# Kernel tuning notes

Measured on AMD Instinct MI355X. Metric: run time of the kernel, lower is better.

The kernel has to match this reference:

```python
import jax, jax.numpy as jnp
import numpy as np

B, E, H, V, T = 64, 512, 1024, 32000, 31  # T = max_len - 1


def _lstm_step(x, h, c, Wx, Wh, b):
    # Keras LSTM with activation=None (linear), recurrent_activation=sigmoid, gate order i,f,g,o
    z = x @ Wx + h @ Wh + b
    i, f, g, o = jnp.split(z, 4, axis=-1)
    c_new = jax.nn.sigmoid(f) * c + jax.nn.sigmoid(i) * g  # g is linear (activation=None)
    h_new = jax.nn.sigmoid(o) * c_new                      # linear activation on cell output
    return h_new, c_new


def setup_inputs() -> dict:
    key = jax.random.key(0)
    k = jax.random.split(key, 6)
    def gl(kk, shape, fan_in):
        return jax.random.normal(kk, shape, dtype=jnp.float32) / np.float32(np.sqrt(fan_in))
    return {
        "inp": jax.random.normal(k[0], (B, 1, E), dtype=jnp.float32),
        "Wx1": gl(k[1], (E, 4 * H), E),
        "Wh1": gl(k[2], (H, 4 * H), H),
        "b1": jnp.zeros((4 * H,), jnp.float32),
        "Wx2": gl(k[3], (H, 4 * H), H),
        "Wh2": gl(k[4], (H, 4 * H), H),
        "b2": jnp.zeros((4 * H,), jnp.float32),
        "Wd": gl(k[5], (H, V), H),
        "bd": jnp.zeros((V,), jnp.float32),
    }


def reference(inp, Wx1, Wh1, b1, Wx2, Wh2, b2, Wd, bd):
    Bk = inp.shape[0]
    h = jnp.zeros((Bk, H), inp.dtype)
    c = jnp.zeros((Bk, H), inp.dtype)

    # encoder LSTM over the (length-1) input sequence, zero initial state
    def enc(carry, x):
        h, c = carry
        h, c = _lstm_step(x, h, c, Wx1, Wh1, b1)
        return (h, c), None
    (h, c), _ = jax.lax.scan(enc, (h, c), jnp.swapaxes(inp, 0, 1))  # time-major (T_in,B,E)

    key = jax.random.key(1234)

    # decode loop: lstm_rest consumes its own previous output (== previous state_h)
    def dec(carry, t):
        h, c = carry
        h2, c2 = _lstm_step(h, h, c, Wx2, Wh2, b2)
        logp = jax.nn.log_softmax(h2 @ Wd + bd, axis=-1)  # Dense(softmax) -> Categorical(probs)
        probs = jnp.exp(logp)
        kk = jax.random.fold_in(key, t)
        sample = jax.random.categorical(kk, logp, axis=-1)                    # dist.sample()
        log_prob = jnp.take_along_axis(logp, sample[:, None], axis=1)[:, 0]   # dist.log_prob
        ent = -jnp.sum(probs * logp, axis=-1)                                 # dist.entropy
        return (h2, c2), (sample, log_prob, ent)

    (h, c), (msg, lp, ent) = jax.lax.scan(dec, (h, c), jnp.arange(T))

    def pad(a):  # (T,B) -> (B,T) then concat zeros along axis 1 -> (B,2T)
        a = a.T
        return jnp.concatenate([a, jnp.zeros_like(a)], axis=1)

    return pad(msg), pad(lp), pad(ent), h
```

## Files before the change

kernel.cpp:

```cpp
#include <hip/hip_runtime.h>
#include <stdint.h>
#include <math.h>

#define B_DIM 64
#define E_DIM 512
#define H_DIM 1024
#define V_DIM 32000
#define T_STEPS 31
#define GATES 4096
#define OUT_COLS 62
#define NCHUNK 125
#define STOT 32
#define NTPAIR 16
#define NBLK2 (NTPAIR * NCHUNK)

#define RNG_PARTITIONABLE 1

typedef _Float16 half8 __attribute__((ext_vector_type(8)));
typedef float floatx4 __attribute__((ext_vector_type(4)));

__device__ __forceinline__ void tf_round(uint32_t& x0, uint32_t& x1, int r) {
  x0 += x1;
  x1 = (x1 << r) | (x1 >> (32 - r));
  x1 ^= x0;
}

__device__ __forceinline__ void threefry2x32(uint32_t k0, uint32_t k1,
                                             uint32_t& x0, uint32_t& x1) {
  uint32_t k2 = k0 ^ k1 ^ 0x1BD11BDAu;
  x0 += k0; x1 += k1;
  tf_round(x0,x1,13); tf_round(x0,x1,15); tf_round(x0,x1,26); tf_round(x0,x1,6);
  x0 += k1; x1 += k2 + 1u;
  tf_round(x0,x1,17); tf_round(x0,x1,29); tf_round(x0,x1,16); tf_round(x0,x1,24);
  x0 += k2; x1 += k0 + 2u;
  tf_round(x0,x1,13); tf_round(x0,x1,15); tf_round(x0,x1,26); tf_round(x0,x1,6);
  x0 += k0; x1 += k1 + 3u;
  tf_round(x0,x1,17); tf_round(x0,x1,29); tf_round(x0,x1,16); tf_round(x0,x1,24);
  x0 += k1; x1 += k2 + 4u;
  tf_round(x0,x1,13); tf_round(x0,x1,15); tf_round(x0,x1,26); tf_round(x0,x1,6);
  x0 += k2; x1 += k0 + 5u;
}

__global__ void zero_kernel(float* __restrict__ o, int n) {
  int i = blockIdx.x * blockDim.x + threadIdx.x;
  if (i < n) o[i] = 0.0f;
}

__global__ void copy_kernel(const float* __restrict__ a, float* __restrict__ o, int n) {
  int i = blockIdx.x * blockDim.x + threadIdx.x;
  if (i < n) o[i] = a[i];
}

__global__ __launch_bounds__(256)
void repack_w(const float* __restrict__ Wa, const float* __restrict__ Wb,
              _Float16* __restrict__ pk, int N) {
  int gw = blockIdx.x * 4 + (threadIdx.x >> 6);
  int total = (N >> 4) * STOT;
  if (gw >= total) return;
  int nt = gw >> 5, s = gw & 31;
  int lane = threadIdx.x & 63;
  int quad = lane >> 4, lm = lane & 15;
  int col = nt * 16 + lm;
  half8 hi, lo;
#pragma unroll
  for (int j = 0; j < 8; ++j) {
    int row = s * 32 + quad * 8 + j;
    float v = Wa[(size_t)row * N + col];
    if (Wb) v += Wb[(size_t)row * N + col];
    _Float16 h = (_Float16)v;
    hi[j] = h;
    lo[j] = (_Float16)(v - (float)h);
  }
  _Float16* o = pk + ((size_t)(nt * 32 + s) * 2) * 512 + lane * 8;
  *(half8*)o = hi;
  *(half8*)(o + 512) = lo;
}

#define LOAD_FRAGS(s_, A_, B_)                                              \
  {                                                                         \
    _Pragma("unroll")                                                       \
    for (int mt = 0; mt < 4; ++mt) {                                        \
      const half8* ap = Apk + ((size_t)(mt * 32 + (s_)) * 2) * 64 + lane;   \
      A_[mt][0] = ap[0];                                                    \
      A_[mt][1] = ap[64];                                                   \
    }                                                                       \
    _Pragma("unroll")                                                       \
    for (int nt = 0; nt < 4; ++nt) {                                        \
      const half8* bp =                                                     \
          Wpk + ((size_t)((nt0 + nt) * 32 + (s_)) * 2) * 64 + lane;         \
      B_[nt][0] = bp[0];                                                    \
      B_[nt][1] = bp[64];                                                   \
    }                                                                       \
  }

#define DO_MFMA(A_, B_)                                                     \
  {                                                                         \
    _Pragma("unroll")                                                       \
    for (int mt = 0; mt < 4; ++mt) {                                        \
      _Pragma("unroll")                                                     \
      for (int nt = 0; nt < 4; ++nt) {                                      \
        acc[mt][nt] = __builtin_amdgcn_mfma_f32_16x16x32_f16(               \
            A_[mt][0], B_[nt][0], acc[mt][nt], 0, 0, 0);                    \
        acc[mt][nt] = __builtin_amdgcn_mfma_f32_16x16x32_f16(               \
            A_[mt][1], B_[nt][0], acc[mt][nt], 0, 0, 0);                    \
        acc[mt][nt] = __builtin_amdgcn_mfma_f32_16x16x32_f16(               \
            A_[mt][0], B_[nt][1], acc[mt][nt], 0, 0, 0);                    \
      }                                                                     \
    }                                                                       \
  }

__global__ __launch_bounds__(256, 1)
void mfma_gemm(const half8* __restrict__ Apk, const half8* __restrict__ Wpk,
               float* __restrict__ P, int N) {
  const int w = threadIdx.x >> 6;
  const int lane = threadIdx.x & 63;
  const int schunk = STOT / gridDim.y;
  const int s0 = blockIdx.y * schunk;
  const int send = s0 + schunk;
  const int nt0 = blockIdx.x * 16 + w * 4;

  floatx4 acc[4][4] = {};
  half8 a0[4][2], b0[4][2], a1[4][2], b1[4][2];

  LOAD_FRAGS(s0, a0, b0);
  for (int s = s0; s < send; s += 2) {
    LOAD_FRAGS(s + 1, a1, b1);
    DO_MFMA(a0, b0);
    if (s + 2 < send) LOAD_FRAGS(s + 2, a0, b0);
    DO_MFMA(a1, b1);
  }

  const int row0 = (lane >> 4) * 4;
  const int colb = blockIdx.x * 256 + w * 64 + (lane & 15);
  float* Pb = P + (size_t)blockIdx.y * 64 * N;
#pragma unroll
  for (int mt = 0; mt < 4; ++mt)
#pragma unroll
    for (int nt = 0; nt < 4; ++nt)
#pragma unroll
      for (int r = 0; r < 4; ++r)
        Pb[(size_t)(mt * 16 + row0 + r) * N + colb + nt * 16] = acc[mt][nt][r];
}

__global__ __launch_bounds__(512, 2)
void mfma_logits_fused(const half8* __restrict__ hpkA, const half8* __restrict__ Wpk,
                       const float* __restrict__ bd,
                       float* __restrict__ pm, float* __restrict__ ps,
                       float* __restrict__ pt2, float* __restrict__ pbest,
                       float* __restrict__ plb, int* __restrict__ pbi) {
  const int p = blockIdx.x;
  const int g = (p & 7) * 250 + (p >> 3);
  const int tpair = g & 15;
  const int chunk = g >> 4;

  const int tid = threadIdx.x;
  const int w4 = tid >> 6;
  const int th = w4 >> 2;
  const int w  = w4 & 3;
  const int lane = tid & 63;
  const int lm = lane & 15, q = lane >> 4;
  const int t = tpair * 2 + th;
  const bool active = (t < T_STEPS);
  const int nt0 = chunk * 16 + w * 4;

  floatx4 acc[4][4] = {};

  if (active) {
    const half8* Apk = hpkA + (size_t)(t + 1) * 16384;
    half8 a0[4][2], b0[4][2], a1[4][2], b1[4][2];

    LOAD_FRAGS(0, a0, b0);
    for (int s = 0; s < STOT; s += 2) {
      LOAD_FRAGS(s + 1, a1, b1);
      DO_MFMA(a0, b0);
      if (s + 2 < STOT) LOAD_FRAGS(s + 2, a0, b0);
      DO_MFMA(a1, b1);
    }
  }

  __shared__ float redM[2][4][64];
  __shared__ float redS[2][4][64], redT[2][4][64], redBV[2][4][64], redBL[2][4][64];
  __shared__ int   redBI[2][4][64];

  const int colb = chunk * 256 + w * 64 + lm;
  float M[4][4];

  if (active) {
    float bdv[4];
#pragma unroll
    for (int nt = 0; nt < 4; ++nt) bdv[nt] = bd[colb + nt * 16];
#pragma unroll
    for (int mt = 0; mt < 4; ++mt)
#pragma unroll
      for (int nt = 0; nt < 4; ++nt)
#pragma unroll
        for (int r = 0; r < 4; ++r) acc[mt][nt][r] += bdv[nt];

#pragma unroll
    for (int mt = 0; mt < 4; ++mt) {
#pragma unroll
      for (int r = 0; r < 4; ++r) {
        float m = fmaxf(fmaxf(acc[mt][0][r], acc[mt][1][r]),
                        fmaxf(acc[mt][2][r], acc[mt][3][r]));
#pragma unroll
        for (int off = 1; off <= 8; off <<= 1) m = fmaxf(m, __shfl_xor(m, off));
        if (lm == 0) redM[th][w][mt * 16 + q * 4 + r] = m;
      }
    }
  }
  __syncthreads();

  if (active) {
#pragma unroll
    for (int mt = 0; mt < 4; ++mt)
#pragma unroll
      for (int r = 0; r < 4; ++r) {
        int b = mt * 16 + q * 4 + r;
        M[mt][r] = fmaxf(fmaxf(redM[th][0][b], redM[th][1][b]),
                         fmaxf(redM[th][2][b], redM[th][3][b]));
      }

    uint32_t tk0 = 0u, tk1 = (uint32_t)t;
    threefry2x32(0u, 1234u, tk0, tk1);

#pragma unroll
    for (int mt = 0; mt < 4; ++mt) {
#pragma unroll
      for (int r = 0; r < 4; ++r) {
        const int b = mt * 16 + q * 4 + r;
        const float Mrow = M[mt][r];
        float s = 0.f, t2 = 0.f, bv = -INFINITY, bl = 0.f;
        int bi = 0x7fffffff;
#pragma unroll
        for (int nt = 0; nt < 4; ++nt) {
          float l = acc[mt][nt][r];
          int v = colb + nt * 16;
          float e = __expf(l - Mrow);
          s += e;
          t2 += e * l;
          uint32_t j = (uint32_t)(b * V_DIM + v);
#if RNG_PARTITIONABLE
          uint32_t y0 = 0u, y1 = j;
          threefry2x32(tk0, tk1, y0, y1);
          uint32_t bits = y0 ^ y1;
#else
          const uint32_t half = (uint32_t)(B_DIM * V_DIM / 2);
          uint32_t y0, y1;
          if (j < half) { y0 = j; y1 = j + half; } else { y0 = j - half; y1 = j; }
          threefry2x32(tk0, tk1, y0, y1);
          uint32_t bits = (j < half) ? y0 : y1;
#endif
          float u = __uint_as_float((bits >> 9) | 0x3f800000u) - 1.0f;
          u = fmaxf(u, 1.17549435e-38f);
          float g2 = -__logf(-__logf(u));
          float val = l + g2;
          if (val > bv || (val == bv && v < bi)) { bv = val; bi = v; bl = l; }
        }
#pragma unroll
        for (int off = 1; off <= 8; off <<= 1) {
          s  += __shfl_xor(s, off);
          t2 += __shfl_xor(t2, off);
          float ob = __shfl_xor(bv, off);
          int   oi = __shfl_xor(bi, off);
          float ol = __shfl_xor(bl, off);
          if (ob > bv || (ob == bv && oi < bi)) { bv = ob; bi = oi; bl = ol; }
        }
        if (lm == 0) {
          redS[th][w][b] = s; redT[th][w][b] = t2;
          redBV[th][w][b] = bv; redBI[th][w][b] = bi; redBL[th][w][b] = bl;
        }
      }
    }
  }
  __syncthreads();

  if (active && w == 0) {
    int b = lane;
    float Mg = fmaxf(fmaxf(redM[th][0][b], redM[th][1][b]),
                     fmaxf(redM[th][2][b], redM[th][3][b]));
    float S  = redS[th][0][b] + redS[th][1][b] + redS[th][2][b] + redS[th][3][b];
    float T2 = redT[th][0][b] + redT[th][1][b] + redT[th][2][b] + redT[th][3][b];
    float Bv = redBV[th][0][b]; int BI = redBI[th][0][b]; float Bl = redBL[th][0][b];
#pragma unroll
    for (int ww = 1; ww < 4; ++ww) {
      if (redBV[th][ww][b] > Bv || (redBV[th][ww][b] == Bv && redBI[th][ww][b] < BI)) {
        Bv = redBV[th][ww][b]; BI = redBI[th][ww][b]; Bl = redBL[th][ww][b];
      }
    }
    size_t o = ((size_t)t * B_DIM + b) * NCHUNK + chunk;
    pm[o] = Mg; ps[o] = S; pt2[o] = T2; pbest[o] = Bv; plb[o] = Bl;
    pbi[o] = BI;
  }
}
#undef LOAD_FRAGS
#undef DO_MFMA

__global__ __launch_bounds__(256, 2)
void gemm64_kernel(const float* __restrict__ A, const float* __restrict__ W,
                   float* __restrict__ P, int K, int N) {
  const int vt = blockIdx.x;
  const int ks = blockIdx.y;
  const int kchunk = K / gridDim.y;
  const int kbase = ks * kchunk;
  const int v0 = vt * 256;

  __shared__ float As[32][68];
  __shared__ float Ws[32][256];

  float acc[8][8];
#pragma unroll
  for (int i = 0; i < 8; i++)
#pragma unroll
    for (int j = 0; j < 8; j++) acc[i][j] = 0.0f;

  const int tid = threadIdx.x;
  const int cg4 = (tid & 31) * 4;
  const int rg4 = (tid >> 5) * 4;

  for (int k0 = kbase; k0 < kbase + kchunk; k0 += 32) {
    __syncthreads();
    {
      int b  = tid >> 3;
      int f4 = tid & 7;
      const float* Ab = A + (size_t)b * K + k0 + f4 * 4;
      float4 a0 = *(const float4*)Ab;
      float4 a1 = *(const float4*)(Ab + (size_t)32 * K);
      int kk0 = f4 * 4;
      As[kk0+0][b] = a0.x; As[kk0+1][b] = a0.y; As[kk0+2][b] = a0.z; As[kk0+3][b] = a0.w;
      As[kk0+0][b+32] = a1.x; As[kk0+1][b+32] = a1.y; As[kk0+2][b+32] = a1.z; As[kk0+3][b+32] = a1.w;
    }
#pragma unroll
    for (int p = 0; p < 8; p++) {
      int idx = tid + p * 256;
      int row = idx >> 6, c4 = idx & 63;
      *(float4*)&Ws[row][c4 * 4] =
          *(const float4*)(W + (size_t)(k0 + row) * N + v0 + c4 * 4);
    }
    __syncthreads();

#pragma unroll 8
    for (int kk = 0; kk < 32; kk++) {
      float4 a0 = *(const float4*)&As[kk][rg4];
      float4 a1 = *(const float4*)&As[kk][32 + rg4];
      float4 w0 = *(const float4*)&Ws[kk][cg4];
      float4 w1 = *(const float4*)&Ws[kk][128 + cg4];
      float av[8] = {a0.x, a0.y, a0.z, a0.w, a1.x, a1.y, a1.z, a1.w};
      float wv[8] = {w0.x, w0.y, w0.z, w0.w, w1.x, w1.y, w1.z, w1.w};
#pragma unroll
      for (int i = 0; i < 8; i++)
#pragma unroll
        for (int j = 0; j < 8; j++)
          acc[i][j] = fmaf(av[i], wv[j], acc[i][j]);
    }
  }

  const size_t base = (size_t)ks * 64 * N;
#pragma unroll
  for (int i = 0; i < 8; i++) {
    int row = (i < 4) ? (rg4 + i) : (32 + rg4 + i - 4);
    float4 s0 = make_float4(acc[i][0], acc[i][1], acc[i][2], acc[i][3]);
    float4 s1 = make_float4(acc[i][4], acc[i][5], acc[i][6], acc[i][7]);
    *(float4*)(P + base + (size_t)row * N + v0 + cg4) = s0;
    *(float4*)(P + base + (size_t)row * N + v0 + 128 + cg4) = s1;
  }
}

__global__ void gates_kernel(const float* __restrict__ zp, int ksplit,
                             const float* __restrict__ bias,
                             const float* __restrict__ c_in,
                             float* __restrict__ h_out, float* __restrict__ c_out,
                             _Float16* __restrict__ hpk) {
  int tid = blockIdx.x * blockDim.x + threadIdx.x;
  if (tid >= B_DIM * H_DIM) return;
  int b = tid >> 10, j = tid & 1023;
  float zi = bias[j], zf = bias[j + 1024], zg = bias[j + 2048], zo = bias[j + 3072];
  const float* Pb = zp + (size_t)b * GATES;
  for (int p = 0; p < ksplit; p++) {
    const float* P = Pb + (size_t)p * B_DIM * GATES;
    zi += P[j]; zf += P[j + 1024]; zg += P[j + 2048]; zo += P[j + 3072];
  }
  float cp = c_in ? c_in[tid] : 0.0f;
  float si = 1.0f / (1.0f + expf(-zi));
  float sf = 1.0f / (1.0f + expf(-zf));
  float so = 1.0f / (1.0f + expf(-zo));
  float c = sf * cp + si * zg;
  c_out[tid] = c;
  float hv = so * c;
  h_out[tid] = hv;

  int mt = b >> 4, lm = b & 15;
  int s = j >> 5, quad = (j >> 3) & 3, jj = j & 7;
  size_t off = ((size_t)(mt * 32 + s) * 2) * 512 + (size_t)(quad * 16 + lm) * 8 + jj;
  _Float16 hh = (_Float16)hv;
  hpk[off] = hh;
  hpk[off + 512] = (_Float16)(hv - (float)hh);
}

__global__ __launch_bounds__(128)
void sample_stage2_batch(const float* __restrict__ pm, const float* __restrict__ ps,
                         const float* __restrict__ pt2, const float* __restrict__ pbest,
                         const float* __restrict__ plb, const int* __restrict__ pbi,
                         float* __restrict__ out) {
  const int b = blockIdx.x;
  const int t = blockIdx.y;
  const int tid = threadIdx.x;
  const size_t base = ((size_t)t * B_DIM + b) * NCHUNK;
  const bool valid = tid < NCHUNK;

  float m   = valid ? pm[base + tid]    : -INFINITY;
  float bv  = valid ? pbest[base + tid] : -INFINITY;
  float blv = valid ? plb[base + tid]   : 0.0f;
  int   bi  = valid ? pbi[base + tid]   : 0x7fffffff;

  float M = m;
  for (int off = 32; off > 0; off >>= 1) M = fmaxf(M, __shfl_down(M, off));
  __shared__ float sM[2];
  int wave = tid >> 6, lane = tid & 63;
  if (lane == 0) sM[wave] = M;
  __syncthreads();
  const float Mg = fmaxf(sM[0], sM[1]);

  float sc = valid ? expf(m - Mg) : 0.0f;
  float s  = valid ? ps[base + tid]  * sc : 0.0f;
  float t2 = valid ? pt2[base + tid] * sc : 0.0f;
  for (int off = 32; off > 0; off >>= 1) {
    s  += __shfl_down(s, off);
    t2 += __shfl_down(t2, off);
    float ob = __shfl_down(bv, off);
    int   oi = __shfl_down(bi, off);
    float ol = __shfl_down(blv, off);
    if (ob > bv || (ob == bv && oi < bi)) { bv = ob; bi = oi; blv = ol; }
  }
  __shared__ float sS[2], sT[2], sB[2], sL[2];
  __shared__ int sI[2];
  if (lane == 0) { sS[wave] = s; sT[wave] = t2; sB[wave] = bv; sI[wave] = bi; sL[wave] = blv; }
  __syncthreads();
  if (tid == 0) {
    float S = sS[0] + sS[1], T2 = sT[0] + sT[1];
    float Bv = sB[0], Bl = sL[0]; int BI = sI[0];
    if (sB[1] > Bv || (sB[1] == Bv && sI[1] < BI)) { Bv = sB[1]; BI = sI[1]; Bl = sL[1]; }
    float lse = Mg + logf(S);
    out[(size_t)b * OUT_COLS + t]        = (float)BI;
    out[3968 + (size_t)b * OUT_COLS + t] = Bl - lse;
    out[7936 + (size_t)b * OUT_COLS + t] = lse - T2 / S;
  }
}

extern "C" void kernel_launch(void* const* d_in, const int* in_sizes, int n_in,
                              void* d_out, int out_size, void* d_ws, size_t ws_size,
                              hipStream_t stream) {
  const float* inp = (const float*)d_in[0];
  const float* Wx1 = (const float*)d_in[1];
  const float* b1  = (const float*)d_in[3];
  const float* Wx2 = (const float*)d_in[4];
  const float* Wh2 = (const float*)d_in[5];
  const float* b2  = (const float*)d_in[6];
  const float* Wd  = (const float*)d_in[7];
  const float* bd  = (const float*)d_in[8];
  float* out = (float*)d_out;

  float* ws = (float*)d_ws;
  float* Wd_pk  = ws;
  float* W2_pk  = Wd_pk + 32768000;
  float* hpkA   = W2_pk + 4194304;
  float* zparts = hpkA + 2097152;
  float* h      = zparts + 2097152;
  float* c      = h + 65536;

  float* pm    = zparts;
  float* ps    = zparts + 248000;
  float* pt2   = zparts + 496000;
  float* pbest = zparts + 744000;
  float* plb   = zparts + 992000;
  int*   pbi   = (int*)(zparts + 1240000);

  repack_w<<<16000, 256, 0, stream>>>(Wd, nullptr, (_Float16*)Wd_pk, V_DIM);
  repack_w<<<2048, 256, 0, stream>>>(Wx2, Wh2, (_Float16*)W2_pk, GATES);
  zero_kernel<<<47, 256, 0, stream>>>(out, 11904);

  gemm64_kernel<<<dim3(16, 4), 256, 0, stream>>>(inp, Wx1, zparts, E_DIM, GATES);
  gates_kernel<<<256, 256, 0, stream>>>(zparts, 4, b1, nullptr, h, c,
                                        (_Float16*)hpkA);

  for (int t = 0; t < T_STEPS; t++) {
    mfma_gemm<<<dim3(16, 8), 256, 0, stream>>>(
        (const half8*)(hpkA + (size_t)t * 65536), (const half8*)W2_pk,
        zparts, GATES);
    gates_kernel<<<256, 256, 0, stream>>>(
        zparts, 8, b2, c, h, c, (_Float16*)(hpkA + (size_t)(t + 1) * 65536));
  }

  mfma_logits_fused<<<dim3(NBLK2), 512, 0, stream>>>(
      (const half8*)hpkA, (const half8*)Wd_pk, bd,
      pm, ps, pt2, pbest, plb, pbi);

  sample_stage2_batch<<<dim3(B_DIM, T_STEPS), 128, 0, stream>>>(
      pm, ps, pt2, pbest, plb, pbi, out);

  copy_kernel<<<256, 256, 0, stream>>>(h, out + 11904, B_DIM * H_DIM);
}
```

Baseline: 1.353 ms.

## Fuse recurrent LSTM GEMM with gate activation into one per-step kernel

Replaces the per-step split-K MFMA GEMM plus separate gates kernel with a single kernel. Each block computes all four gate columns for 16 hidden units and 32 batch rows, reduces its two K-halves through shared-memory atomics, then applies the LSTM cell update and writes the packed fp16 hi/lo state for the next step. This removes one launch per step and the global round trip of the 8-way partial sums. In exchange the per-block work and occupancy layout change (128 blocks of 512 threads), and the weight tiles are re-read by both batch halves.

```diff
diff --git a/kernel.cpp b/kernel.cpp
--- a/kernel.cpp
+++ b/kernel.cpp
@@ -109,37 +109,102 @@
     }                                                                       \
   }
 
-__global__ __launch_bounds__(256, 1)
-void mfma_gemm(const half8* __restrict__ Apk, const half8* __restrict__ Wpk,
-               float* __restrict__ P, int N) {
-  const int w = threadIdx.x >> 6;
-  const int lane = threadIdx.x & 63;
-  const int schunk = STOT / gridDim.y;
-  const int s0 = blockIdx.y * schunk;
-  const int send = s0 + schunk;
-  const int nt0 = blockIdx.x * 16 + w * 4;
-
-  floatx4 acc[4][4] = {};
-  half8 a0[4][2], b0[4][2], a1[4][2], b1[4][2];
-
-  LOAD_FRAGS(s0, a0, b0);
-  for (int s = s0; s < send; s += 2) {
-    LOAD_FRAGS(s + 1, a1, b1);
-    DO_MFMA(a0, b0);
-    if (s + 2 < send) LOAD_FRAGS(s + 2, a0, b0);
-    DO_MFMA(a1, b1);
-  }
-
-  const int row0 = (lane >> 4) * 4;
-  const int colb = blockIdx.x * 256 + w * 64 + (lane & 15);
-  float* Pb = P + (size_t)blockIdx.y * 64 * N;
-#pragma unroll
-  for (int mt = 0; mt < 4; ++mt)
-#pragma unroll
-    for (int nt = 0; nt < 4; ++nt)
-#pragma unroll
-      for (int r = 0; r < 4; ++r)
-        Pb[(size_t)(mt * 16 + row0 + r) * N + colb + nt * 16] = acc[mt][nt][r];
+__global__ __launch_bounds__(512, 2)
+void lstm_step_fused(const half8* __restrict__ Apk,
+                     const half8* __restrict__ Wpk,
+                     const float* __restrict__ bias,
+                     float* __restrict__ c,
+                     float* __restrict__ h_out,
+                     _Float16* __restrict__ hpk_next)
+{
+  const int x = blockIdx.x;
+  const int mhalf = blockIdx.y;
+  const int tid = threadIdx.x;
+  const int wv = tid >> 6;
+  const int quad = wv >> 1;
+  const int spart = wv & 1;
+  const int lane = tid & 63;
+
+  __shared__ float zsm[32][68];
+
+  for (int i = tid; i < 32 * 68; i += 512) ((float*)zsm)[i] = 0.0f;
+  __syncthreads();
+
+  const int nt = quad * 64 + x;
+  floatx4 acc[2] = {};
+  half8 a0[2][2], b0[2], a1[2][2], b1[2];
+
+#define LF2(s_, A_, B_)                                                        \
+  {                                                                            \
+    _Pragma("unroll")                                                          \
+    for (int i = 0; i < 2; ++i) {                                              \
+      const half8* ap =                                                        \
+          Apk + ((size_t)((mhalf * 2 + i) * 32 + (s_)) * 2) * 64 + lane;       \
+      A_[i][0] = ap[0];                                                        \
+      A_[i][1] = ap[64];                                                       \
+    }                                                                          \
+    const half8* bp = Wpk + ((size_t)(nt * 32 + (s_)) * 2) * 64 + lane;        \
+    B_[0] = bp[0];                                                             \
+    B_[1] = bp[64];                                                            \
+  }
+
+#define MM2(A_, B_)                                                            \
+  {                                                                            \
+    _Pragma("unroll")                                                          \
+    for (int i = 0; i < 2; ++i) {                                              \
+      acc[i] = __builtin_amdgcn_mfma_f32_16x16x32_f16(A_[i][0], B_[0],         \
+                                                      acc[i], 0, 0, 0);        \
+      acc[i] = __builtin_amdgcn_mfma_f32_16x16x32_f16(A_[i][1], B_[0],         \
+                                                      acc[i], 0, 0, 0);        \
+      acc[i] = __builtin_amdgcn_mfma_f32_16x16x32_f16(A_[i][0], B_[1],         \
+                                                      acc[i], 0, 0, 0);        \
+    }                                                                          \
+  }
+
+  const int s0 = spart * 16;
+  LF2(s0, a0, b0);
+  for (int s = s0; s < s0 + 16; s += 2) {
+    LF2(s + 1, a1, b1);
+    MM2(a0, b0);
+    if (s + 2 < s0 + 16) LF2(s + 2, a0, b0);
+    MM2(a1, b1);
+  }
+#undef LF2
+#undef MM2
+
+  const int cm = lane & 15, rq = lane >> 4;
+#pragma unroll
+  for (int i = 0; i < 2; ++i)
+#pragma unroll
+    for (int r = 0; r < 4; ++r)
+      atomicAdd(&zsm[i * 16 + rq * 4 + r][quad * 16 + cm], acc[i][r]);
+  __syncthreads();
+
+  const int bl = tid >> 4;
+  const int b = mhalf * 32 + bl;
+  const int hl = tid & 15;
+  const int j = x * 16 + hl;
+
+  float zi = bias[j]        + zsm[bl][hl];
+  float zf = bias[j + 1024] + zsm[bl][16 + hl];
+  float zg = bias[j + 2048] + zsm[bl][32 + hl];
+  float zo = bias[j + 3072] + zsm[bl][48 + hl];
+
+  float cp = c[(size_t)b * H_DIM + j];
+  float si = 1.0f / (1.0f + expf(-zi));
+  float sf = 1.0f / (1.0f + expf(-zf));
+  float so = 1.0f / (1.0f + expf(-zo));
+  float cn = sf * cp + si * zg;
+  c[(size_t)b * H_DIM + j] = cn;
+  float hv = so * cn;
+  h_out[(size_t)b * H_DIM + j] = hv;
+
+  int mt = b >> 4, lm = b & 15;
+  int s = j >> 5, q2 = (j >> 3) & 3, jj = j & 7;
+  size_t off = ((size_t)(mt * 32 + s) * 2) * 512 + (size_t)(q2 * 16 + lm) * 8 + jj;
+  _Float16 hh = (_Float16)hv;
+  hpk_next[off] = hh;
+  hpk_next[off + 512] = (_Float16)(hv - (float)hh);
 }
 
 __global__ __launch_bounds__(512, 2)
@@ -483,11 +548,9 @@
                                         (_Float16*)hpkA);
 
   for (int t = 0; t < T_STEPS; t++) {
-    mfma_gemm<<<dim3(16, 8), 256, 0, stream>>>(
+    lstm_step_fused<<<dim3(64, 2), 512, 0, stream>>>(
         (const half8*)(hpkA + (size_t)t * 65536), (const half8*)W2_pk,
-        zparts, GATES);
-    gates_kernel<<<256, 256, 0, stream>>>(
-        zparts, 8, b2, c, h, c, (_Float16*)(hpkA + (size_t)(t + 1) * 65536));
+        b2, c, h, (_Float16*)(hpkA + (size_t)(t + 1) * 65536));
   }
 
   mfma_logits_fused<<<dim3(NBLK2), 512, 0, stream>>>(
```

Result: no change. 1.371 ms (+1.3%).

## Replace per-step LSTM GEMM and gate launches with one persistent grid-synced kernel

Applied to the files above, without the earlier changes.

The 31 decoder steps used to launch a split-K MFMA GEMM plus a gates kernel each, with partial sums round-tripping through global memory. A single persistent kernel of 128 blocks now does the full-K GEMM for its tile, applies the gates in shared memory, keeps the cell state in registers, and writes packed fp16 hi/lo h for the next step. Steps are separated by an atomic-counter grid barrier. This removes about 62 launches and the partial-sum traffic, at the cost of barrier latency, less parallelism per step (no split-K), and reliance on all 128 blocks being resident at once.

```diff
diff --git a/kernel.cpp b/kernel.cpp
--- a/kernel.cpp
+++ b/kernel.cpp
@@ -13,6 +13,7 @@
 #define STOT 32
 #define NTPAIR 16
 #define NBLK2 (NTPAIR * NCHUNK)
+#define REC_NBLK 128
 
 #define RNG_PARTITIONABLE 1
 
@@ -74,6 +75,112 @@
   _Float16* o = pk + ((size_t)(nt * 32 + s) * 2) * 512 + lane * 8;
   *(half8*)o = hi;
   *(half8*)(o + 512) = lo;
+}
+
+__device__ __forceinline__ void grid_sync(int* bar, int epoch, int nblk) {
+  __syncthreads();
+  if (threadIdx.x == 0) {
+    __threadfence();
+    int prev = __hip_atomic_fetch_add(&bar[0], 1, __ATOMIC_ACQ_REL,
+                                      __HIP_MEMORY_SCOPE_AGENT);
+    if (prev == nblk - 1) {
+      __hip_atomic_store(&bar[0], 0, __ATOMIC_RELAXED, __HIP_MEMORY_SCOPE_AGENT);
+      __hip_atomic_store(&bar[1], epoch, __ATOMIC_RELEASE, __HIP_MEMORY_SCOPE_AGENT);
+    } else {
+      while (__hip_atomic_load(&bar[1], __ATOMIC_ACQUIRE,
+                               __HIP_MEMORY_SCOPE_AGENT) < epoch)
+        __builtin_amdgcn_s_sleep(2);
+    }
+    __threadfence();
+  }
+  __syncthreads();
+}
+
+__global__ __launch_bounds__(512, 1)
+void lstm_persistent(const half8* __restrict__ hpkA, const half8* __restrict__ Wpk,
+                     const float* __restrict__ bias,
+                     const float* __restrict__ c_in,
+                     float* __restrict__ h_out,
+                     _Float16* __restrict__ hpk_base,
+                     int* __restrict__ bar) {
+  const int x = blockIdx.x;
+  const int mhalf = blockIdx.y;
+  const int tid = threadIdx.x;
+  const int wv = tid >> 6;
+  const int mtl = wv & 1;
+  const int q = wv >> 1;
+  const int mt = mhalf * 2 + mtl;
+  const int nt = q * 64 + x;
+  const int lane = tid & 63;
+  const int cm = lane & 15, rq = lane >> 4;
+
+  __shared__ float zsm[32][68];
+
+  const int row_l = tid >> 4;
+  const int grow = mhalf * 32 + row_l;
+  const int hl = tid & 15;
+  const int j = x * 16 + hl;
+  const float bi_ = bias[j], bf_ = bias[j + 1024];
+  const float bg_ = bias[j + 2048], bo_ = bias[j + 3072];
+  float cp = c_in[(size_t)grow * H_DIM + j];
+
+  const int mtp = grow >> 4, lmp = grow & 15;
+  const int sp = j >> 5, q2 = (j >> 3) & 3, jj = j & 7;
+  const size_t off_in_slot =
+      ((size_t)(mtp * 32 + sp) * 2) * 512 + (size_t)(q2 * 16 + lmp) * 8 + jj;
+
+#define LFP(s_, AH, AL, BH, BL)                                              \
+  {                                                                          \
+    const half8* ap_ = Apk + ((size_t)(mt * 32 + (s_)) * 2) * 64 + lane;     \
+    AH = ap_[0]; AL = ap_[64];                                               \
+    const half8* bp_ = Wpk + ((size_t)(nt * 32 + (s_)) * 2) * 64 + lane;     \
+    BH = bp_[0]; BL = bp_[64];                                               \
+  }
+#define MMP(AH, AL, BH, BL)                                                  \
+  {                                                                          \
+    acc = __builtin_amdgcn_mfma_f32_16x16x32_f16(AH, BH, acc, 0, 0, 0);      \
+    acc = __builtin_amdgcn_mfma_f32_16x16x32_f16(AL, BH, acc, 0, 0, 0);      \
+    acc = __builtin_amdgcn_mfma_f32_16x16x32_f16(AH, BL, acc, 0, 0, 0);      \
+  }
+
+  for (int t = 0; t < T_STEPS; ++t) {
+    const half8* Apk = hpkA + (size_t)t * 16384;
+    floatx4 acc = {};
+    half8 a0h, a0l, b0h, b0l, a1h, a1l, b1h, b1l;
+
+    LFP(0, a0h, a0l, b0h, b0l);
+    for (int s = 0; s < STOT; s += 2) {
+      LFP(s + 1, a1h, a1l, b1h, b1l);
+      MMP(a0h, a0l, b0h, b0l);
+      if (s + 2 < STOT) LFP(s + 2, a0h, a0l, b0h, b0l);
+      MMP(a1h, a1l, b1h, b1l);
+    }
+
+#pragma unroll
+    for (int r = 0; r < 4; ++r)
+      zsm[mtl * 16 + rq * 4 + r][q * 16 + cm] = acc[r];
+    __syncthreads();
+
+    float zi = bi_ + zsm[row_l][hl];
+    float zf = bf_ + zsm[row_l][16 + hl];
+    float zg = bg_ + zsm[row_l][32 + hl];
+    float zo = bo_ + zsm[row_l][48 + hl];
+    float si = 1.0f / (1.0f + expf(-zi));
+    float sf = 1.0f / (1.0f + expf(-zf));
+    float so = 1.0f / (1.0f + expf(-zo));
+    cp = sf * cp + si * zg;
+    float hv = so * cp;
+    if (t == T_STEPS - 1) h_out[(size_t)grow * H_DIM + j] = hv;
+
+    _Float16* hp = hpk_base + (size_t)(t + 1) * 131072 + off_in_slot;
+    _Float16 hh = (_Float16)hv;
+    hp[0] = hh;
+    hp[512] = (_Float16)(hv - (float)hh);
+
+    if (t < T_STEPS - 1) grid_sync(bar, t + 1, REC_NBLK);
+  }
+#undef LFP
+#undef MMP
 }
 
 #define LOAD_FRAGS(s_, A_, B_)                                              \
@@ -108,39 +215,6 @@
       }                                                                     \
     }                                                                       \
   }
-
-__global__ __launch_bounds__(256, 1)
-void mfma_gemm(const half8* __restrict__ Apk, const half8* __restrict__ Wpk,
-               float* __restrict__ P, int N) {
-  const int w = threadIdx.x >> 6;
-  const int lane = threadIdx.x & 63;
-  const int schunk = STOT / gridDim.y;
-  const int s0 = blockIdx.y * schunk;
-  const int send = s0 + schunk;
-  const int nt0 = blockIdx.x * 16 + w * 4;
-
-  floatx4 acc[4][4] = {};
-  half8 a0[4][2], b0[4][2], a1[4][2], b1[4][2];
-
-  LOAD_FRAGS(s0, a0, b0);
-  for (int s = s0; s < send; s += 2) {
-    LOAD_FRAGS(s + 1, a1, b1);
-    DO_MFMA(a0, b0);
-    if (s + 2 < send) LOAD_FRAGS(s + 2, a0, b0);
-    DO_MFMA(a1, b1);
-  }
-
-  const int row0 = (lane >> 4) * 4;
-  const int colb = blockIdx.x * 256 + w * 64 + (lane & 15);
-  float* Pb = P + (size_t)blockIdx.y * 64 * N;
-#pragma unroll
-  for (int mt = 0; mt < 4; ++mt)
-#pragma unroll
-    for (int nt = 0; nt < 4; ++nt)
-#pragma unroll
-      for (int r = 0; r < 4; ++r)
-        Pb[(size_t)(mt * 16 + row0 + r) * N + colb + nt * 16] = acc[mt][nt][r];
-}
 
 __global__ __launch_bounds__(512, 2)
 void mfma_logits_fused(const half8* __restrict__ hpkA, const half8* __restrict__ Wpk,
@@ -466,6 +540,7 @@
   float* zparts = hpkA + 2097152;
   float* h      = zparts + 2097152;
   float* c      = h + 65536;
+  int*   bar    = (int*)(c + 65536);
 
   float* pm    = zparts;
   float* ps    = zparts + 248000;
@@ -477,18 +552,15 @@
   repack_w<<<16000, 256, 0, stream>>>(Wd, nullptr, (_Float16*)Wd_pk, V_DIM);
   repack_w<<<2048, 256, 0, stream>>>(Wx2, Wh2, (_Float16*)W2_pk, GATES);
   zero_kernel<<<47, 256, 0, stream>>>(out, 11904);
+  zero_kernel<<<1, 64, 0, stream>>>((float*)bar, 8);
 
   gemm64_kernel<<<dim3(16, 4), 256, 0, stream>>>(inp, Wx1, zparts, E_DIM, GATES);
   gates_kernel<<<256, 256, 0, stream>>>(zparts, 4, b1, nullptr, h, c,
                                         (_Float16*)hpkA);
 
-  for (int t = 0; t < T_STEPS; t++) {
-    mfma_gemm<<<dim3(16, 8), 256, 0, stream>>>(
-        (const half8*)(hpkA + (size_t)t * 65536), (const half8*)W2_pk,
-        zparts, GATES);
-    gates_kernel<<<256, 256, 0, stream>>>(
-        zparts, 8, b2, c, h, c, (_Float16*)(hpkA + (size_t)(t + 1) * 65536));
-  }
+  lstm_persistent<<<dim3(64, 2), 512, 0, stream>>>(
+      (const half8*)hpkA, (const half8*)W2_pk, b2, c, h,
+      (_Float16*)hpkA, bar);
 
   mfma_logits_fused<<<dim3(NBLK2), 512, 0, stream>>>(
       (const half8*)hpkA, (const half8*)Wd_pk, bd,
```

Measured after the change: 1.701 ms. 25.8% more time.
